# Optimization experiments

Hardware: AMD Instinct MI355X
Metric: run time of the kernel (lower is better)

## Reference

```python
import jax, jax.numpy as jnp
import numpy as np

B = 32768
D_IN = 512
D_OUT = 512
N_DIGITS = 9
N_LEVELS = N_DIGITS + 1


def _xavier_uniform(key, shape, gain):
    # nn.init.xavier_uniform_ on Linear weight of shape (out, in)
    fan_out, fan_in = shape
    limit = gain * np.sqrt(6.0 / (fan_in + fan_out))
    return jax.random.uniform(key, shape, jnp.float32, -limit, limit)


def setup_inputs() -> dict:
    key = jax.random.key(0)
    kx, kv, *kw = jax.random.split(key, 2 + N_LEVELS)
    x = jax.random.normal(kx, (B, D_IN), dtype=jnp.float32)
    valuations = jax.random.randint(kv, (B,), 0, N_LEVELS, dtype=jnp.int64)
    # level-aware xavier init: gain = 1/(1 + 0.1*level)
    W = jnp.stack([
        _xavier_uniform(kw[l], (D_OUT, D_IN), 1.0 / (1.0 + 0.1 * l))
        for l in range(N_LEVELS)
    ], axis=0)  # (L, out, in)
    level_gates = jnp.ones((N_LEVELS,), dtype=jnp.float32)
    cross_level_attn = (jnp.eye(N_LEVELS, dtype=jnp.float32) * 0.9
                        + jnp.ones((N_LEVELS, N_LEVELS), dtype=jnp.float32) * 0.01)
    bias = jnp.zeros((D_OUT,), dtype=jnp.float32)
    return {"x": x, "valuations": valuations, "W": W,
            "level_gates": level_gates, "cross_level_attn": cross_level_attn,
            "bias": bias}


def reference(x, valuations, W, level_gates, cross_level_attn, bias):
    val = jnp.clip(valuations, 0, N_DIGITS)  # (B,)
    # 10 per-level linears as one batched GEMM: (B, L, out)
    level_outputs = jnp.einsum('bi,loi->blo', x, W)
    gates = jax.nn.sigmoid(level_gates)  # (L,)
    level_outputs = level_outputs * gates[None, :, None]
    # per-sample gather of own valuation level -> (B, out)
    output = jnp.take_along_axis(level_outputs, val[:, None, None], axis=1)[:, 0, :]
    # soft cross-level attention combine
    attn_weights = jax.nn.softmax(cross_level_attn[val], axis=-1)  # (B, L)
    weighted = jnp.einsum('bl,blo->bo', attn_weights, level_outputs)
    output = 0.7 * output + 0.3 * weighted
    return output + bias
```

## Files before the change

### kernel.cpp

```cpp
#include <hip/hip_runtime.h>

#define B_N 32768
#define D 512
#define DD (D * D)
#define NLEV 10
#define TM 128
#define TN 256
#define BK 32
#define NITER (D / BK)
#define NHB 128
#define MROWS_MAX 34048
#define MAX_RT (MROWS_MAX / TM)

typedef unsigned short u16;
typedef short s16x8 __attribute__((ext_vector_type(8)));
typedef u16 u16x8 __attribute__((ext_vector_type(8)));
typedef float f32x4 __attribute__((ext_vector_type(4)));

__device__ __forceinline__ u16 f2bf(float f) {
  union { float f; unsigned u; } v; v.f = f;
  unsigned r = v.u + 0x7fffu + ((v.u >> 16) & 1u);
  return (u16)(r >> 16);
}
__device__ __forceinline__ int clampv(int v) {
  return v < 0 ? 0 : (v > NLEV - 1 ? NLEV - 1 : v);
}

__global__ void k1(const float* __restrict__ W, const float* __restrict__ lg,
                   const float* __restrict__ attn, const int* __restrict__ val,
                   u16* __restrict__ weff, u16* __restrict__ hist,
                   int* __restrict__ perm) {
  const int t = threadIdx.x;
  if (blockIdx.x < DD / 256) {
    __shared__ float c[NLEV * NLEV];
    if (t < NLEV) {
      float g[NLEV], a[NLEV], mx = -1e30f;
      #pragma unroll
      for (int l = 0; l < NLEV; ++l) {
        g[l] = 1.0f / (1.0f + expf(-lg[l]));
        a[l] = attn[t * NLEV + l];
        mx = fmaxf(mx, a[l]);
      }
      float s = 0.f;
      #pragma unroll
      for (int l = 0; l < NLEV; ++l) { a[l] = expf(a[l] - mx); s += a[l]; }
      float inv = 1.0f / s;
      #pragma unroll
      for (int l = 0; l < NLEV; ++l) {
        float cc = 0.3f * a[l] * inv * g[l];
        if (l == t) cc += 0.7f * g[t];
        c[t * NLEV + l] = cc;
      }
    }
    __syncthreads();
    const int idx = blockIdx.x * 256 + t;
    float w[NLEV];
    #pragma unroll
    for (int l = 0; l < NLEV; ++l) w[l] = W[l * DD + idx];
    #pragma unroll
    for (int v = 0; v < NLEV; ++v) {
      float s = 0.f;
      #pragma unroll
      for (int l = 0; l < NLEV; ++l) s += c[v * NLEV + l] * w[l];
      weff[v * DD + idx] = f2bf(s);
    }
  } else {
    __shared__ int lc[NLEV];
    const int b = blockIdx.x - DD / 256;
    if (t < NLEV) lc[t] = 0;
    __syncthreads();
    const int gid = b * 256 + t;
    atomicAdd(&lc[clampv(val[gid])], 1);
    perm[gid] = -1;
    if (b < (MROWS_MAX - B_N) / 256) perm[B_N + b * 256 + t] = -1;
    __syncthreads();
    if (t < NLEV) hist[b * NLEV + t] = (u16)lc[t];
  }
}

__global__ void k2(const int* __restrict__ val, const u16* __restrict__ hist,
                   int* __restrict__ perm, int* __restrict__ starts) {
  __shared__ int h[NHB * NLEV];
  __shared__ int st[NLEV + 1];
  __shared__ int cnt[NLEV];
  __shared__ int lc[NLEV];
  const int t = threadIdx.x, b = blockIdx.x;
  for (int i = t; i < NHB * NLEV; i += 256) h[i] = hist[i];
  if (t < NLEV) lc[t] = 0;
  __syncthreads();
  if (t < NLEV) {
    int run = 0;
    for (int bb = 0; bb < NHB; ++bb) {
      int x = h[bb * NLEV + t];
      h[bb * NLEV + t] = run;
      run += x;
    }
    cnt[t] = run;
  }
  __syncthreads();
  if (t == 0) {
    int s = 0;
    for (int v = 0; v < NLEV; ++v) {
      st[v] = s;
      s += (cnt[v] + TM - 1) & ~(TM - 1);
    }
    st[NLEV] = s;
  }
  __syncthreads();
  const int gid = b * 256 + t;
  const int v = clampv(val[gid]);
  const int pos = atomicAdd(&lc[v], 1);
  perm[st[v] + h[b * NLEV + v] + pos] = gid;
  if (b == 0 && t <= NLEV) starts[t] = st[t];
}

__global__ __launch_bounds__(512, 4) void k3(
    const float* __restrict__ x, const u16* __restrict__ weff,
    const int* __restrict__ perm, const int* __restrict__ starts,
    const float* __restrict__ bias, float* __restrict__ out) {
  __shared__ u16 As[2][TM * BK];
  __shared__ u16 Bs[2][TN * BK];

  const int ct = blockIdx.x, rt = blockIdx.y;
  const int Mpad = starts[NLEV];
  if (rt * TM >= Mpad) return;

  int v = 0;
  #pragma unroll
  for (int i = 1; i < NLEV; ++i) if (rt * TM >= starts[i]) v = i;

  const int tid = threadIdx.x;
  const int lane = tid & 63, wave = tid >> 6;
  const int wm = (wave >> 2) * 64, wn = (wave & 3) * 64;
  const int fm = lane & 15;
  const int cb = lane >> 4;

  const int ar = tid >> 2;
  const int ah = tid & 3;
  int prow = perm[rt * TM + ar];
  if (prow < 0) prow = 0;
  const float* xrow = x + (size_t)prow * D + ah * 8;
  const int sw = (ar >> 1) & 3;
  const int aslot = ar * BK + ((ah ^ sw) << 3);

  const u16* wb = weff + ((size_t)v * D + ct * TN) * D;
  const int c0i = wave * 64 + lane;
  const int c1i = 512 + c0i;
  const int n0 = c0i >> 2, s0 = c0i & 3, kc0 = s0 ^ ((n0 >> 1) & 3);
  const int n1 = c1i >> 2, s1 = c1i & 3, kc1 = s1 ^ ((n1 >> 1) & 3);
  const u16* gb0 = wb + n0 * D + kc0 * 8;
  const u16* gb1 = wb + n1 * D + kc1 * 8;
  const int bdst0 = c0i * 8, bdst1 = c1i * 8;

  f32x4 acc[4][4];
  #pragma unroll
  for (int i = 0; i < 4; ++i)
    #pragma unroll
    for (int j = 0; j < 4; ++j) acc[i][j] = (f32x4){0.f, 0.f, 0.f, 0.f};

  {
    __builtin_amdgcn_global_load_lds(
        (const __attribute__((address_space(1))) void*)gb0,
        (__attribute__((address_space(3))) void*)(Bs[0] + bdst0), 16, 0, 0);
    __builtin_amdgcn_global_load_lds(
        (const __attribute__((address_space(1))) void*)gb1,
        (__attribute__((address_space(3))) void*)(Bs[0] + bdst1), 16, 0, 0);
    const f32x4* xp = (const f32x4*)xrow;
    f32x4 f0 = xp[0], f1 = xp[1];
    u16x8 cc;
    #pragma unroll
    for (int q = 0; q < 4; ++q) { cc[q] = f2bf(f0[q]); cc[4 + q] = f2bf(f1[q]); }
    *(u16x8*)(As[0] + aslot) = cc;
  }
  f32x4 cf0, cf1;
  {
    const f32x4* xp = (const f32x4*)(xrow + BK);
    cf0 = xp[0]; cf1 = xp[1];
  }
  __syncthreads();

  int p = 0;
  for (int i = 0; i < NITER; ++i) {
    const bool hn = (i + 1 < NITER);
    if (hn) {
      const int k1o = (i + 1) * BK;
      __builtin_amdgcn_global_load_lds(
          (const __attribute__((address_space(1))) void*)(gb0 + k1o),
          (__attribute__((address_space(3))) void*)(Bs[p ^ 1] + bdst0), 16, 0, 0);
      __builtin_amdgcn_global_load_lds(
          (const __attribute__((address_space(1))) void*)(gb1 + k1o),
          (__attribute__((address_space(3))) void*)(Bs[p ^ 1] + bdst1), 16, 0, 0);
    }
    f32x4 nf0, nf1;
    if (i + 2 < NITER) {
      const f32x4* xp = (const f32x4*)(xrow + (i + 2) * BK);
      nf0 = xp[0]; nf1 = xp[1];
    }
    s16x8 af[4], bf[4];
    #pragma unroll
    for (int t4 = 0; t4 < 4; ++t4) {
      const int m = wm + t4 * 16 + fm;
      af[t4] = *(const s16x8*)(As[p] + m * BK + ((cb ^ ((m >> 1) & 3)) << 3));
      const int n = wn + t4 * 16 + fm;
      bf[t4] = *(const s16x8*)(Bs[p] + n * BK + ((cb ^ ((n >> 1) & 3)) << 3));
    }
    #pragma unroll
    for (int tm = 0; tm < 4; ++tm)
      #pragma unroll
      for (int tn = 0; tn < 4; ++tn)
        acc[tm][tn] = __builtin_amdgcn_mfma_f32_16x16x32_bf16(af[tm], bf[tn], acc[tm][tn], 0, 0, 0);
    if (hn) {
      u16x8 cc;
      #pragma unroll
      for (int q = 0; q < 4; ++q) { cc[q] = f2bf(cf0[q]); cc[4 + q] = f2bf(cf1[q]); }
      *(u16x8*)(As[p ^ 1] + aslot) = cc;
      cf0 = nf0; cf1 = nf1;
    }
    __syncthreads();
    p ^= 1;
  }

  float bv[4];
  #pragma unroll
  for (int tn = 0; tn < 4; ++tn) bv[tn] = bias[ct * TN + wn + tn * 16 + fm];
  #pragma unroll
  for (int tm = 0; tm < 4; ++tm) {
    #pragma unroll
    for (int r = 0; r < 4; ++r) {
      const int mrow = wm + tm * 16 + (lane >> 4) * 4 + r;
      const int p2 = perm[rt * TM + mrow];
      if (p2 >= 0) {
        float* o = out + (size_t)p2 * D + ct * TN + wn + fm;
        #pragma unroll
        for (int tn = 0; tn < 4; ++tn)
          o[tn * 16] = acc[tm][tn][r] + bv[tn];
      }
    }
  }
}

extern "C" void kernel_launch(void* const* d_in, const int* in_sizes, int n_in,
                              void* d_out, int out_size, void* d_ws, size_t ws_size,
                              hipStream_t stream) {
  const float* x    = (const float*)d_in[0];
  const int*   val  = (const int*)d_in[1];
  const float* W    = (const float*)d_in[2];
  const float* lg   = (const float*)d_in[3];
  const float* attn = (const float*)d_in[4];
  const float* bias = (const float*)d_in[5];
  float* out = (float*)d_out;

  char* ws = (char*)d_ws;
  int* starts = (int*)(ws + 0);
  u16* hist   = (u16*)(ws + 64);
  int* perm   = (int*)(ws + 2688);
  u16* weff   = (u16*)(ws + 139264);

  k1<<<DD / 256 + NHB, 256, 0, stream>>>(W, lg, attn, val, weff, hist, perm);
  k2<<<NHB, 256, 0, stream>>>(val, hist, perm, starts);
  k3<<<dim3(D / TN, MAX_RT), 512, 0, stream>>>(x, weff, perm, starts, bias, out);
}
```

Baseline: 174.6 us.

## Stream fp32 activations directly into LDS and convert to bf16 at fragment load

The A operand (gathered x rows) is now copied as fp32 straight into LDS with asynchronous global_load_lds, replacing the register prefetch plus software bf16 rounding and LDS store. The bf16 conversion moves to fragment-load time using the hardware packed convert instruction, with a new XOR swizzle for the fp32 layout. The loop also switches to explicit waitcnt plus barrier and raises wave priority around the MFMA block. The costs are double the LDS footprint for A, more LDS read traffic, and the conversion being repeated by every wave that reads the same rows. Rounding may also differ slightly from the old manual round-to-nearest-even.

```diff
diff --git a/kernel.cpp b/kernel.cpp
--- a/kernel.cpp
+++ b/kernel.cpp
@@ -118,8 +118,8 @@
     const float* __restrict__ x, const u16* __restrict__ weff,
     const int* __restrict__ perm, const int* __restrict__ starts,
     const float* __restrict__ bias, float* __restrict__ out) {
-  __shared__ u16 As[2][TM * BK];
-  __shared__ u16 Bs[2][TN * BK];
+  __shared__ float Asf[2][TM * BK];
+  __shared__ u16   Bsu[2][TN * BK];
 
   const int ct = blockIdx.x, rt = blockIdx.y;
   const int Mpad = starts[NLEV];
@@ -135,13 +135,16 @@
   const int fm = lane & 15;
   const int cb = lane >> 4;
 
-  const int ar = tid >> 2;
-  const int ah = tid & 3;
-  int prow = perm[rt * TM + ar];
-  if (prow < 0) prow = 0;
-  const float* xrow = x + (size_t)prow * D + ah * 8;
-  const int sw = (ar >> 1) & 3;
-  const int aslot = ar * BK + ((ah ^ sw) << 3);
+  const int arow = tid >> 3;
+  const int kch = (tid & 7) ^ (arow & 7);
+  int pr0 = perm[rt * TM + arow];
+  int pr1 = perm[rt * TM + 64 + arow];
+  if (pr0 < 0) pr0 = 0;
+  if (pr1 < 0) pr1 = 0;
+  const float* ga0 = x + (size_t)pr0 * D + kch * 4;
+  const float* ga1 = x + (size_t)pr1 * D + kch * 4;
+  const int adst0 = tid * 4;
+  const int adst1 = (512 + tid) * 4;
 
   const u16* wb = weff + ((size_t)v * D + ct * TN) * D;
   const int c0i = wave * 64 + lane;
@@ -152,71 +155,78 @@
   const u16* gb1 = wb + n1 * D + kc1 * 8;
   const int bdst0 = c0i * 8, bdst1 = c1i * 8;
 
+  const int sl0 = (2 * cb) ^ (fm & 7);
+  const int sl1 = (2 * cb + 1) ^ (fm & 7);
+
   f32x4 acc[4][4];
   #pragma unroll
   for (int i = 0; i < 4; ++i)
     #pragma unroll
     for (int j = 0; j < 4; ++j) acc[i][j] = (f32x4){0.f, 0.f, 0.f, 0.f};
 
-  {
-    __builtin_amdgcn_global_load_lds(
-        (const __attribute__((address_space(1))) void*)gb0,
-        (__attribute__((address_space(3))) void*)(Bs[0] + bdst0), 16, 0, 0);
-    __builtin_amdgcn_global_load_lds(
-        (const __attribute__((address_space(1))) void*)gb1,
-        (__attribute__((address_space(3))) void*)(Bs[0] + bdst1), 16, 0, 0);
-    const f32x4* xp = (const f32x4*)xrow;
-    f32x4 f0 = xp[0], f1 = xp[1];
-    u16x8 cc;
-    #pragma unroll
-    for (int q = 0; q < 4; ++q) { cc[q] = f2bf(f0[q]); cc[4 + q] = f2bf(f1[q]); }
-    *(u16x8*)(As[0] + aslot) = cc;
-  }
-  f32x4 cf0, cf1;
-  {
-    const f32x4* xp = (const f32x4*)(xrow + BK);
-    cf0 = xp[0]; cf1 = xp[1];
-  }
-  __syncthreads();
+  __builtin_amdgcn_global_load_lds(
+      (const __attribute__((address_space(1))) void*)ga0,
+      (__attribute__((address_space(3))) void*)(Asf[0] + adst0), 16, 0, 0);
+  __builtin_amdgcn_global_load_lds(
+      (const __attribute__((address_space(1))) void*)ga1,
+      (__attribute__((address_space(3))) void*)(Asf[0] + adst1), 16, 0, 0);
+  __builtin_amdgcn_global_load_lds(
+      (const __attribute__((address_space(1))) void*)gb0,
+      (__attribute__((address_space(3))) void*)(Bsu[0] + bdst0), 16, 0, 0);
+  __builtin_amdgcn_global_load_lds(
+      (const __attribute__((address_space(1))) void*)gb1,
+      (__attribute__((address_space(3))) void*)(Bsu[0] + bdst1), 16, 0, 0);
+  asm volatile("s_waitcnt vmcnt(0)" ::: "memory");
+  __builtin_amdgcn_s_barrier();
+  __builtin_amdgcn_sched_barrier(0);
 
   int p = 0;
   for (int i = 0; i < NITER; ++i) {
     const bool hn = (i + 1 < NITER);
     if (hn) {
-      const int k1o = (i + 1) * BK;
-      __builtin_amdgcn_global_load_lds(
-          (const __attribute__((address_space(1))) void*)(gb0 + k1o),
-          (__attribute__((address_space(3))) void*)(Bs[p ^ 1] + bdst0), 16, 0, 0);
-      __builtin_amdgcn_global_load_lds(
-          (const __attribute__((address_space(1))) void*)(gb1 + k1o),
-          (__attribute__((address_space(3))) void*)(Bs[p ^ 1] + bdst1), 16, 0, 0);
-    }
-    f32x4 nf0, nf1;
-    if (i + 2 < NITER) {
-      const f32x4* xp = (const f32x4*)(xrow + (i + 2) * BK);
-      nf0 = xp[0]; nf1 = xp[1];
-    }
+      const int ko = (i + 1) * BK;
+      __builtin_amdgcn_global_load_lds(
+          (const __attribute__((address_space(1))) void*)(ga0 + ko),
+          (__attribute__((address_space(3))) void*)(Asf[p ^ 1] + adst0), 16, 0, 0);
+      __builtin_amdgcn_global_load_lds(
+          (const __attribute__((address_space(1))) void*)(ga1 + ko),
+          (__attribute__((address_space(3))) void*)(Asf[p ^ 1] + adst1), 16, 0, 0);
+      __builtin_amdgcn_global_load_lds(
+          (const __attribute__((address_space(1))) void*)(gb0 + ko),
+          (__attribute__((address_space(3))) void*)(Bsu[p ^ 1] + bdst0), 16, 0, 0);
+      __builtin_amdgcn_global_load_lds(
+          (const __attribute__((address_space(1))) void*)(gb1 + ko),
+          (__attribute__((address_space(3))) void*)(Bsu[p ^ 1] + bdst1), 16, 0, 0);
+    }
+    const float* Af = (const float*)Asf[p];
     s16x8 af[4], bf[4];
     #pragma unroll
     for (int t4 = 0; t4 < 4; ++t4) {
       const int m = wm + t4 * 16 + fm;
-      af[t4] = *(const s16x8*)(As[p] + m * BK + ((cb ^ ((m >> 1) & 3)) << 3));
+      const f32x4 lo = *(const f32x4*)(Af + m * 32 + sl0 * 4);
+      const f32x4 hi = *(const f32x4*)(Af + m * 32 + sl1 * 4);
+      union { unsigned w[4]; s16x8 v; } u;
+      asm("v_cvt_pk_bf16_f32 %0, %1, %2" : "=v"(u.w[0]) : "v"(lo[0]), "v"(lo[1]));
+      asm("v_cvt_pk_bf16_f32 %0, %1, %2" : "=v"(u.w[1]) : "v"(lo[2]), "v"(lo[3]));
+      asm("v_cvt_pk_bf16_f32 %0, %1, %2" : "=v"(u.w[2]) : "v"(hi[0]), "v"(hi[1]));
+      asm("v_cvt_pk_bf16_f32 %0, %1, %2" : "=v"(u.w[3]) : "v"(hi[2]), "v"(hi[3]));
+      af[t4] = u.v;
       const int n = wn + t4 * 16 + fm;
-      bf[t4] = *(const s16x8*)(Bs[p] + n * BK + ((cb ^ ((n >> 1) & 3)) << 3));
-    }
+      bf[t4] = *(const s16x8*)(Bsu[p] + n * BK + ((cb ^ ((n >> 1) & 3)) << 3));
+    }
+    __builtin_amdgcn_s_setprio(1);
     #pragma unroll
     for (int tm = 0; tm < 4; ++tm)
       #pragma unroll
       for (int tn = 0; tn < 4; ++tn)
         acc[tm][tn] = __builtin_amdgcn_mfma_f32_16x16x32_bf16(af[tm], bf[tn], acc[tm][tn], 0, 0, 0);
+    __builtin_amdgcn_s_setprio(0);
     if (hn) {
-      u16x8 cc;
-      #pragma unroll
-      for (int q = 0; q < 4; ++q) { cc[q] = f2bf(cf0[q]); cc[4 + q] = f2bf(cf1[q]); }
-      *(u16x8*)(As[p ^ 1] + aslot) = cc;
-      cf0 = nf0; cf1 = nf1;
-    }
-    __syncthreads();
+      asm volatile("s_waitcnt vmcnt(0)" ::: "memory");
+      asm volatile("s_waitcnt lgkmcnt(0)" ::: "memory");
+      __builtin_amdgcn_s_barrier();
+      __builtin_amdgcn_sched_barrier(0);
+    }
     p ^= 1;
   }
 
```

Result: no change. 177.6 us (+1.7%).
